# Kernel optimization log

Hardware: AMD Instinct MI355X
Metric: run time of the kernel (lower is better)

## Reference

```python
import jax, jax.numpy as jnp
import numpy as np

N, E, IN, HID, EE, L, NB = 20000, 256000, 64, 128, 32, 3, 8


def _silu(x):
    return x * jax.nn.sigmoid(x)


def setup_inputs() -> dict:
    key = jax.random.key(0)
    ks = list(jax.random.split(key, 32))

    def nrm(k, shape, fan_in):
        return jax.random.normal(k, shape, dtype=jnp.float32) / np.sqrt(fan_in)

    inp = {}
    inp["H_t"] = jax.random.normal(ks[0], (N, IN), dtype=jnp.float32)
    inp["X_t"] = jax.random.normal(ks[1], (N, 3), dtype=jnp.float32)
    inp["cond_embedding"] = jax.random.normal(ks[2], (N, HID), dtype=jnp.float32)
    inp["t"] = jax.random.uniform(ks[3], (N,), dtype=jnp.float32)
    inp["edges"] = jax.random.randint(ks[4], (2, E), 0, N)
    inp["edge_types"] = jax.random.randint(ks[5], (E,), 0, 2)
    inp["generate_mask"] = jax.random.bernoulli(ks[6], 0.7, (N,))
    inp["batch_ids"] = jnp.sort(jax.random.randint(ks[7], (N,), 0, NB))
    # input MLP: (IN + 2*HID) -> HID -> HID -> HID, 3 linear layers
    d0 = IN + 2 * HID
    inp["mlp_W0"] = nrm(ks[8], (d0, HID), d0)
    inp["mlp_b0"] = jnp.zeros((HID,), jnp.float32)
    inp["mlp_W1"] = nrm(ks[9], (HID, HID), HID)
    inp["mlp_b1"] = jnp.zeros((HID,), jnp.float32)
    inp["mlp_W2"] = nrm(ks[10], (HID, HID), HID)
    inp["mlp_b2"] = jnp.zeros((HID,), jnp.float32)
    inp["edge_table"] = jax.random.normal(ks[11], (2, EE), dtype=jnp.float32)
    # encoder (EGNN-style message passing), stacked over L layers
    de = 2 * HID + 1 + EE  # [h_src, h_dst, dist^2, edge_embed]
    inp["We"] = nrm(ks[12], (L, de, HID), de)
    inp["be"] = jnp.zeros((L, HID), jnp.float32)
    inp["Wx"] = nrm(ks[13], (L, HID, 1), HID)
    inp["bx"] = jnp.zeros((L, 1), jnp.float32)
    inp["Wh"] = nrm(ks[14], (L, 2 * HID, HID), 2 * HID)
    inp["bh"] = jnp.zeros((L, HID), jnp.float32)
    inp["h2i_W"] = nrm(ks[15], (HID, IN), HID)
    inp["h2i_b"] = jnp.zeros((IN,), jnp.float32)
    return inp


def reference(H_t, X_t, cond_embedding, t, mlp_W0, mlp_b0, mlp_W1, mlp_b1,
              mlp_W2, mlp_b2, edge_table, We, be, Wx, bx, Wh, bh,
              h2i_W, h2i_b, edges, edge_types, generate_mask, batch_ids):
    n = H_t.shape[0]
    hid = mlp_W2.shape[1]
    # sinusoidal time embedding (dim = hidden_size)
    half = hid // 2
    freqs = jnp.exp(jnp.arange(half, dtype=jnp.float32) * (-np.log(10000.0) / (half - 1)))
    ang = t[:, None] * freqs[None, :]
    t_embed = jnp.concatenate([jnp.sin(ang), jnp.cos(ang)], axis=-1)  # (N, hid)
    # input MLP
    feat = jnp.concatenate([H_t, cond_embedding, t_embed], axis=-1)
    h = jax.nn.relu(feat @ mlp_W0 + mlp_b0)
    h = jax.nn.relu(h @ mlp_W1 + mlp_b1)
    h = h @ mlp_W2 + mlp_b2
    eemb = edge_table[edge_types]  # (E, EE)
    src, dst = edges[0], edges[1]
    cnt = jax.ops.segment_sum(jnp.ones((src.shape[0], 1), h.dtype), dst, num_segments=n)
    x = X_t
    for l in range(We.shape[0]):
        diff = x[src] - x[dst]                              # (E, 3)
        d2 = jnp.sum(diff * diff, axis=-1, keepdims=True)   # (E, 1)
        m_in = jnp.concatenate([h[src], h[dst], d2, eemb], axis=-1)
        msg = _silu(m_in @ We[l] + be[l])                   # (E, hid)
        w = msg @ Wx[l] + bx[l]                             # (E, 1)
        agg_x = jax.ops.segment_sum(diff * w, dst, num_segments=n)
        x = x + agg_x / (cnt + 1.0)
        agg_m = jax.ops.segment_sum(msg, dst, num_segments=n)
        h = h + _silu(jnp.concatenate([h, agg_m], axis=-1) @ Wh[l] + bh[l])
    mask = generate_mask[:, None]
    v_X = jnp.where(mask, x, jnp.zeros_like(x))
    v_H = jnp.where(mask, h @ h2i_W + h2i_b, 0.0)
    return (v_H, v_X)
```

## Files before the change

### kernel.cpp

```cpp
#include <hip/hip_runtime.h>
#include <math.h>

#define NN 20000
#define NE 256000
#define IN_DIM 64
#define HID 128
#define DE 289
#define D0 320
#define TILE_E 64
#define NB64 313
#define NUB 8
#define SRCMASK 0x3FFFFFFF

typedef unsigned short u16;
typedef unsigned int u32;
typedef unsigned long long u64;
typedef __attribute__((ext_vector_type(8))) short short8;
typedef __attribute__((ext_vector_type(4))) float float4v;

#define OFF_WE   0
#define OFF_W0   122880
#define OFF_W1   163840
#define OFF_W2   180224
#define OFF_WH   196608
#define OFF_H2I  294912
#define PACK_TOT 303104
#define PREP_TOT (PACK_TOT + 1152 + NN)

static __device__ __forceinline__ u16 f2bf(float f) {
    unsigned int u = __float_as_uint(f);
    u += 0x7fffu + ((u >> 16) & 1u);
    return (u16)(u >> 16);
}
static __device__ __forceinline__ float bf2f(u16 s) {
    return __uint_as_float(((unsigned int)s) << 16);
}
static __device__ __forceinline__ float bflo(u32 u) { return bf2f((u16)(u & 0xffffu)); }
static __device__ __forceinline__ float bfhi(u32 u) { return bf2f((u16)(u >> 16)); }
static __device__ __forceinline__ u32 pack2(float a, float b) {
    return (u32)f2bf(a) | ((u32)f2bf(b) << 16);
}
static __device__ __forceinline__ uint4 pack8(const float* v) {
    uint4 r;
    r.x = (u32)f2bf(v[0]) | ((u32)f2bf(v[1]) << 16);
    r.y = (u32)f2bf(v[2]) | ((u32)f2bf(v[3]) << 16);
    r.z = (u32)f2bf(v[4]) | ((u32)f2bf(v[5]) << 16);
    r.w = (u32)f2bf(v[6]) | ((u32)f2bf(v[7]) << 16);
    return r;
}
static __device__ __forceinline__ float silu(float v) {
    return v * (1.f / (1.f + __expf(-v)));
}

__global__ __launch_bounds__(256) void hist_kernel(
    const float* __restrict__ X_t, const int* __restrict__ edges,
    float* __restrict__ x, int* __restrict__ deg)
{
    int gid = blockIdx.x * blockDim.x + threadIdx.x;
    int stride = gridDim.x * blockDim.x;
    for (int i = gid; i < NN * 3; i += stride) x[i] = X_t[i];
    for (int e = gid; e < NE; e += stride)
        atomicAdd(&deg[edges[NE + e]], 1);
}

__global__ __launch_bounds__(1024) void scan_kernel(
    const int* __restrict__ deg, int* __restrict__ row_start, int* __restrict__ head)
{
    __shared__ int s[1024];
    int tx = threadIdx.x;
    const int per = (NN + 1023) / 1024;
    int st = tx * per, en = st + per;
    if (st > NN) st = NN;
    if (en > NN) en = NN;
    int sum = 0;
    for (int i = st; i < en; ++i) sum += deg[i];
    s[tx] = sum;
    __syncthreads();
    for (int off = 1; off < 1024; off <<= 1) {
        int t = (tx >= off) ? s[tx - off] : 0;
        __syncthreads();
        s[tx] += t;
        __syncthreads();
    }
    int run = (tx == 0) ? 0 : s[tx - 1];
    for (int i = st; i < en; ++i) {
        row_start[i] = run; head[i] = run; run += deg[i];
    }
    if (tx == 1023) row_start[NN] = run;
}

__global__ __launch_bounds__(256) void scatter_kernel(
    const int* __restrict__ edges, const int* __restrict__ etype,
    int* __restrict__ head,
    int* __restrict__ src_s)
{
    int gid = blockIdx.x * blockDim.x + threadIdx.x;
    int stride = gridDim.x * blockDim.x;
    for (int e = gid; e < NE; e += stride) {
        int d = edges[NE + e];
        int p = atomicAdd(&head[d], 1);
        src_s[p] = edges[e] | (etype[e] << 30);
    }
}

__global__ __launch_bounds__(256) void prep_kernel(
    const float* __restrict__ We, const float* __restrict__ W0,
    const float* __restrict__ W1, const float* __restrict__ W2,
    const float* __restrict__ Wh, const float* __restrict__ h2i,
    const float* __restrict__ edge_table, const float* __restrict__ be,
    u16* __restrict__ Bp, float* __restrict__ tv, float* __restrict__ wed2,
    int* __restrict__ deg)
{
    int idx = blockIdx.x * 256 + threadIdx.x;
    if (idx < PACK_TOT) {
        const float* src; int N = 128, Ksrc; int r;
        if (idx < OFF_W0) {
            int layer = idx / 40960; r = idx - layer * 40960;
            src = We + (size_t)layer * DE * HID; Ksrc = DE;
        } else if (idx < OFF_W1) { r = idx - OFF_W0; src = W0; Ksrc = 320; }
        else if (idx < OFF_W2)   { r = idx - OFF_W1; src = W1; Ksrc = 128; }
        else if (idx < OFF_WH)   { r = idx - OFF_W2; src = W2; Ksrc = 128; }
        else if (idx < OFF_H2I) {
            int t = idx - OFF_WH; int layer = t / 32768; r = t - layer * 32768;
            src = Wh + (size_t)layer * 256 * HID; Ksrc = 256;
        } else { r = idx - OFF_H2I; src = h2i; Ksrc = 128; N = 64; }
        int ntc = N / 16;
        int j = r & 7, lane = (r >> 3) & 63;
        int rem = r >> 9;
        int nt = rem % ntc, ks = rem / ntc;
        int k = ks * 32 + ((lane >> 4) << 3) + j;
        int c = nt * 16 + (lane & 15);
        Bp[idx] = f2bf((k < Ksrc) ? src[(size_t)k * N + c] : 0.f);
    } else if (idx < PACK_TOT + 768) {
        int q = idx - PACK_TOT;
        int f = q & 127, t = (q >> 7) & 1, l = q >> 8;
        float acc = be[l * 128 + f];
        const float* W = We + (size_t)l * DE * HID;
        #pragma unroll
        for (int k = 0; k < 32; ++k)
            acc += edge_table[t * 32 + k] * W[(size_t)(257 + k) * HID + f];
        tv[l * 256 + t * 128 + f] = acc;
    } else if (idx < PACK_TOT + 1152) {
        int r = idx - PACK_TOT - 768;
        int f = r & 127, l = r >> 7;
        wed2[l * 128 + f] = We[(size_t)l * DE * HID + (size_t)256 * HID + f];
    } else if (idx < PREP_TOT) {
        deg[idx - PACK_TOT - 1152] = 0;
    }
}

__global__ __launch_bounds__(256) void node_mlp_mfma_kernel(
    const float* __restrict__ H_t, const float* __restrict__ cond,
    const float* __restrict__ t_in,
    const u16* __restrict__ W0p, const float* __restrict__ b0,
    const u16* __restrict__ W1p, const float* __restrict__ b1,
    const u16* __restrict__ W2p, const float* __restrict__ b2,
    const u16* __restrict__ WEp,
    u16* __restrict__ Csrc, u16* __restrict__ Cdst,
    float* __restrict__ h, u16* __restrict__ h_bf)
{
    __shared__ u16 s_A[64 * 64];
    __shared__ u16 s_B[64 * 128];
    __shared__ u16 s_h[64 * 128];
    __shared__ float s_t[64];

    int tx = threadIdx.x;
    int n0 = blockIdx.x * 64;
    int l = tx & 63, w = tx >> 6;
    int mt_base = (w & 1) * 2, nt_base = (w >> 1) * 4;
    const float cfr = -logf(10000.f) / 63.f;

    if (tx < 64) s_t[tx] = (n0 + tx < NN) ? t_in[n0 + tx] : 0.f;

    float4v acc[2][4];
    #pragma unroll
    for (int mi = 0; mi < 2; ++mi)
        #pragma unroll
        for (int ni = 0; ni < 4; ++ni) acc[mi][ni] = (float4v){0.f,0.f,0.f,0.f};

    for (int t = 0; t < 5; ++t) {
        __syncthreads();
        #pragma unroll
        for (int it = 0; it < 2; ++it) {
            int flat = it * 256 + tx;
            int n = flat >> 3, sl = flat & 7;
            int c = sl ^ (n & 7);
            int k0 = t * 64 + c * 8;
            float tv8[8];
            int gn = n0 + n;
            if (gn < NN) {
                if (k0 < 192) {
                    const float* src = (k0 < 64) ? &H_t[(size_t)gn * IN_DIM + k0]
                                                 : &cond[(size_t)gn * HID + (k0 - 64)];
                    float4 a = *(const float4*)src;
                    float4 b = *(const float4*)(src + 4);
                    tv8[0]=a.x; tv8[1]=a.y; tv8[2]=a.z; tv8[3]=a.w;
                    tv8[4]=b.x; tv8[5]=b.y; tv8[6]=b.z; tv8[7]=b.w;
                } else {
                    float tvv = s_t[n];
                    int jj = (k0 - 192) & 63;
                    bool is_sin = (k0 < 256);
                    #pragma unroll
                    for (int jx = 0; jx < 8; ++jx) {
                        float ang = tvv * __expf(cfr * (float)(jj + jx));
                        tv8[jx] = is_sin ? __sinf(ang) : __cosf(ang);
                    }
                }
            } else {
                #pragma unroll
                for (int jx = 0; jx < 8; ++jx) tv8[jx] = 0.f;
            }
            *(uint4*)&s_A[n * 64 + sl * 8] = pack8(tv8);
        }
        #pragma unroll
        for (int it = 0; it < 4; ++it) {
            int flat = it * 256 + tx;
            ((uint4*)s_B)[flat] = ((const uint4*)(W0p + (size_t)t * 8192))[flat];
        }
        __syncthreads();
        #pragma unroll
        for (int s = 0; s < 2; ++s) {
            short8 af[2], bfv[4];
            #pragma unroll
            for (int mi = 0; mi < 2; ++mi) {
                int m = (mt_base + mi) * 16 + (l & 15);
                int c = s * 4 + (l >> 4);
                int slot = c ^ (l & 7);
                af[mi] = *(const short8*)(s_A + m * 64 + slot * 8);
            }
            #pragma unroll
            for (int ni = 0; ni < 4; ++ni)
                bfv[ni] = *(const short8*)(s_B + ((s * 8 + nt_base + ni) * 64 + l) * 8);
            #pragma unroll
            for (int mi = 0; mi < 2; ++mi)
                #pragma unroll
                for (int ni = 0; ni < 4; ++ni)
                    acc[mi][ni] = __builtin_amdgcn_mfma_f32_16x16x32_bf16(
                        af[mi], bfv[ni], acc[mi][ni], 0, 0, 0);
        }
    }
    #pragma unroll
    for (int mi = 0; mi < 2; ++mi) {
        #pragma unroll
        for (int ni = 0; ni < 4; ++ni) {
            int f = (nt_base + ni) * 16 + (l & 15);
            float bv = b0[f];
            #pragma unroll
            for (int r = 0; r < 4; ++r) {
                int m = (mt_base + mi) * 16 + (l >> 4) * 4 + r;
                float v = fmaxf(acc[mi][ni][r] + bv, 0.f);
                int slot = (f >> 3) ^ (m & 7);
                s_h[m * 128 + slot * 8 + (f & 7)] = f2bf(v);
            }
            acc[mi][ni] = (float4v){0.f,0.f,0.f,0.f};
        }
    }
    for (int t = 0; t < 2; ++t) {
        __syncthreads();
        #pragma unroll
        for (int it = 0; it < 4; ++it) {
            int flat = it * 256 + tx;
            ((uint4*)s_B)[flat] = ((const uint4*)(W1p + (size_t)t * 8192))[flat];
        }
        __syncthreads();
        #pragma unroll
        for (int s = 0; s < 2; ++s) {
            short8 af[2], bfv[4];
            #pragma unroll
            for (int mi = 0; mi < 2; ++mi) {
                int m = (mt_base + mi) * 16 + (l & 15);
                int c = t * 8 + s * 4 + (l >> 4);
                int slot = c ^ (l & 7);
                af[mi] = *(const short8*)(s_h + m * 128 + slot * 8);
            }
            #pragma unroll
            for (int ni = 0; ni < 4; ++ni)
                bfv[ni] = *(const short8*)(s_B + ((s * 8 + nt_base + ni) * 64 + l) * 8);
            #pragma unroll
            for (int mi = 0; mi < 2; ++mi)
                #pragma unroll
                for (int ni = 0; ni < 4; ++ni)
                    acc[mi][ni] = __builtin_amdgcn_mfma_f32_16x16x32_bf16(
                        af[mi], bfv[ni], acc[mi][ni], 0, 0, 0);
        }
    }
    __syncthreads();
    #pragma unroll
    for (int mi = 0; mi < 2; ++mi) {
        #pragma unroll
        for (int ni = 0; ni < 4; ++ni) {
            int f = (nt_base + ni) * 16 + (l & 15);
            float bv = b1[f];
            #pragma unroll
            for (int r = 0; r < 4; ++r) {
                int m = (mt_base + mi) * 16 + (l >> 4) * 4 + r;
                float v = fmaxf(acc[mi][ni][r] + bv, 0.f);
                int slot = (f >> 3) ^ (m & 7);
                s_h[m * 128 + slot * 8 + (f & 7)] = f2bf(v);
            }
            acc[mi][ni] = (float4v){0.f,0.f,0.f,0.f};
        }
    }
    for (int t = 0; t < 2; ++t) {
        __syncthreads();
        #pragma unroll
        for (int it = 0; it < 4; ++it) {
            int flat = it * 256 + tx;
            ((uint4*)s_B)[flat] = ((const uint4*)(W2p + (size_t)t * 8192))[flat];
        }
        __syncthreads();
        #pragma unroll
        for (int s = 0; s < 2; ++s) {
            short8 af[2], bfv[4];
            #pragma unroll
            for (int mi = 0; mi < 2; ++mi) {
                int m = (mt_base + mi) * 16 + (l & 15);
                int c = t * 8 + s * 4 + (l >> 4);
                int slot = c ^ (l & 7);
                af[mi] = *(const short8*)(s_h + m * 128 + slot * 8);
            }
            #pragma unroll
            for (int ni = 0; ni < 4; ++ni)
                bfv[ni] = *(const short8*)(s_B + ((s * 8 + nt_base + ni) * 64 + l) * 8);
            #pragma unroll
            for (int mi = 0; mi < 2; ++mi)
                #pragma unroll
                for (int ni = 0; ni < 4; ++ni)
                    acc[mi][ni] = __builtin_amdgcn_mfma_f32_16x16x32_bf16(
                        af[mi], bfv[ni], acc[mi][ni], 0, 0, 0);
        }
    }
    __syncthreads();
    #pragma unroll
    for (int mi = 0; mi < 2; ++mi) {
        #pragma unroll
        for (int ni = 0; ni < 4; ++ni) {
            int f = (nt_base + ni) * 16 + (l & 15);
            float bv = b2[f];
            #pragma unroll
            for (int r = 0; r < 4; ++r) {
                int m = (mt_base + mi) * 16 + (l >> 4) * 4 + r;
                int gn = n0 + m;
                float v = acc[mi][ni][r] + bv;
                int slot = (f >> 3) ^ (m & 7);
                s_h[m * 128 + slot * 8 + (f & 7)] = f2bf(v);
                if (gn < NN) {
                    h[(size_t)gn * HID + f] = v;
                    h_bf[(size_t)gn * HID + f] = f2bf(v);
                }
            }
        }
    }

    for (int sd = 0; sd < 2; ++sd) {
        #pragma unroll
        for (int mi = 0; mi < 2; ++mi)
            #pragma unroll
            for (int ni = 0; ni < 4; ++ni) acc[mi][ni] = (float4v){0.f,0.f,0.f,0.f};
        #pragma unroll
        for (int th = 0; th < 2; ++th) {
            int t = sd * 2 + th;
            __syncthreads();
            #pragma unroll
            for (int it = 0; it < 4; ++it) {
                int flat = it * 256 + tx;
                ((uint4*)s_B)[flat] = ((const uint4*)(WEp + (size_t)t * 8192))[flat];
            }
            __syncthreads();
            #pragma unroll
            for (int s = 0; s < 2; ++s) {
                short8 af[2], bfv[4];
                #pragma unroll
                for (int mi = 0; mi < 2; ++mi) {
                    int m = (mt_base + mi) * 16 + (l & 15);
                    int c = th * 8 + s * 4 + (l >> 4);
                    int slot = c ^ (l & 7);
                    af[mi] = *(const short8*)(s_h + m * 128 + slot * 8);
                }
                #pragma unroll
                for (int ni = 0; ni < 4; ++ni)
                    bfv[ni] = *(const short8*)(s_B + ((s * 8 + nt_base + ni) * 64 + l) * 8);
                #pragma unroll
                for (int mi = 0; mi < 2; ++mi)
                    #pragma unroll
                    for (int ni = 0; ni < 4; ++ni)
                        acc[mi][ni] = __builtin_amdgcn_mfma_f32_16x16x32_bf16(
                            af[mi], bfv[ni], acc[mi][ni], 0, 0, 0);
            }
        }
        u16* Cout = (sd == 0) ? Csrc : Cdst;
        #pragma unroll
        for (int mi = 0; mi < 2; ++mi) {
            #pragma unroll
            for (int ni = 0; ni < 4; ++ni) {
                int fq = (nt_base + ni) * 16 + (l & 15);
                #pragma unroll
                for (int r = 0; r < 4; ++r) {
                    int m = (mt_base + mi) * 16 + (l >> 4) * 4 + r;
                    int gn = n0 + m;
                    if (gn < NN)
                        Cout[(size_t)gn * 128 + fq] = f2bf(acc[mi][ni][r]);
                }
            }
        }
    }
}

__global__ __launch_bounds__(512, 4) void node_fused_kernel(
    float* __restrict__ h, u16* __restrict__ h_bf,
    const float* __restrict__ x_in, float* __restrict__ x_out,
    const u16* __restrict__ Csrc, const u16* __restrict__ Cdst,
    u16* __restrict__ Csrc_n, u16* __restrict__ Cdst_n,
    const u16* __restrict__ Wnext, const float* __restrict__ bfin,
    const int* __restrict__ gmask, float* __restrict__ out,
    const int* __restrict__ src_s,
    const int* __restrict__ row_start,
    const float* __restrict__ tv_l, const float* __restrict__ wed2_l,
    const float* __restrict__ Wx_l, const float* __restrict__ bx_l,
    const u16* __restrict__ Whp_l, const float* __restrict__ bh_l,
    int mode)
{
    __shared__ u16 s_A[16 * 256];
    __shared__ u16 s_h2[16 * 128];

    int tx = threadIdx.x;
    int n0 = blockIdx.x * NUB;
    int l = tx & 63, w = tx >> 6;
    int i = w;
    int gn = n0 + i;
    int p = l & 31, q = l >> 5;

    if (tx < 256) {
        int n = tx >> 4, c = tx & 15;
        int slot = c ^ (n & 7);
        uint4 v = make_uint4(0, 0, 0, 0);
        if (n < NUB) v = *(const uint4*)(h_bf + (size_t)(n0 + n) * 128 + c * 8);
        *(uint4*)&s_A[n * 256 + slot * 8] = v;
    } else if (tx < 384) {
        int n = 8 + ((tx - 256) >> 4), c = 16 + (tx & 15);
        int slot = c ^ (n & 7);
        *(uint4*)&s_A[n * 256 + slot * 8] = make_uint4(0, 0, 0, 0);
    }

    float c0[4], d01[4], wed[4], wx[4];
    {
        uint2 cd = *(const uint2*)(Cdst + (size_t)gn * 128 + p * 4);
        float cdv0 = bflo(cd.x), cdv1 = bfhi(cd.x), cdv2 = bflo(cd.y), cdv3 = bfhi(cd.y);
        float4 t0 = *(const float4*)(tv_l + p * 4);
        float4 t1 = *(const float4*)(tv_l + 128 + p * 4);
        float4 wd = *(const float4*)(wed2_l + p * 4);
        float4 wv = *(const float4*)(Wx_l + p * 4);
        c0[0] = t0.x + cdv0; c0[1] = t0.y + cdv1; c0[2] = t0.z + cdv2; c0[3] = t0.w + cdv3;
        d01[0] = t1.x - t0.x; d01[1] = t1.y - t0.y; d01[2] = t1.z - t0.z; d01[3] = t1.w - t0.w;
        wed[0] = wd.x; wed[1] = wd.y; wed[2] = wd.z; wed[3] = wd.w;
        wx[0] = wv.x; wx[1] = wv.y; wx[2] = wv.z; wx[3] = wv.w;
    }
    float bx32 = bx_l[0] * (1.f / 32.f);

    int rs = row_start[gn], re = row_start[gn + 1];
    int d = re - rs;

    float xd0 = x_in[gn * 3 + 0], xd1 = x_in[gn * 3 + 1], xd2 = x_in[gn * 3 + 2];

    float ag[4] = {0.f, 0.f, 0.f, 0.f};
    float sx = 0.f, sy = 0.f, sz = 0.f;

    for (int e0 = 0; e0 < d; e0 += 64) {
        int nchunk = d - e0; if (nchunk > 64) nchunk = 64;
        int sp_l = (l < nchunk) ? src_s[rs + e0 + l] : 0;
        float gx_l = 0.f, gy_l = 0.f, gz_l = 0.f, d2_l = 0.f;
        if (l < nchunk) {
            int sm = sp_l & SRCMASK;
            gx_l = x_in[sm * 3 + 0] - xd0;
            gy_l = x_in[sm * 3 + 1] - xd1;
            gz_l = x_in[sm * 3 + 2] - xd2;
            d2_l = gx_l * gx_l + gy_l * gy_l + gz_l * gz_l;
        }

        auto FETCH = [&](int lj, uint2& cc, float& et) {
            int spE = __shfl(sp_l, lj);
            cc = make_uint2(0u, 0u); et = 0.f;
            if (lj < nchunk) {
                cc = *(const uint2*)(Csrc + (size_t)(spE & SRCMASK) * 128 + p * 4);
                et = (float)((u32)spE >> 30);
            }
        };
        auto PROC = [&](int lj, uint2 cc, float ee) {
            float dxe = __shfl(gx_l, lj);
            float dye = __shfl(gy_l, lj);
            float dze = __shfl(gz_l, lj);
            float d2e = __shfl(d2_l, lj);
            float av[4];
            av[0] = bflo(cc.x); av[1] = bfhi(cc.x);
            av[2] = bflo(cc.y); av[3] = bfhi(cc.y);
            float wpart = bx32;
            #pragma unroll
            for (int f = 0; f < 4; ++f) {
                float t = __fmaf_rn(d2e, wed[f], c0[f]);
                t = __fmaf_rn(ee, d01[f], t);
                float v = av[f] + t;
                float m = silu(v);
                ag[f] += m;
                wpart = __fmaf_rn(m, wx[f], wpart);
            }
            sx = __fmaf_rn(dxe, wpart, sx);
            sy = __fmaf_rn(dye, wpart, sy);
            sz = __fmaf_rn(dze, wpart, sz);
        };

        int ljA = q, ljB = q + 2, ljC = q + 4, ljD = q + 6, ljn = q + 8;
        uint2 ccA, ccB, ccC, ccD; float etA, etB, etC, etD;
        FETCH(ljA, ccA, etA); FETCH(ljB, ccB, etB);
        FETCH(ljC, ccC, etC); FETCH(ljD, ccD, etD);
        while (ljA < nchunk) {
            PROC(ljA, ccA, etA); ljA = ljn; ljn += 2; FETCH(ljA, ccA, etA);
            if (ljB >= nchunk) break;
            PROC(ljB, ccB, etB); ljB = ljn; ljn += 2; FETCH(ljB, ccB, etB);
            if (ljC >= nchunk) break;
            PROC(ljC, ccC, etC); ljC = ljn; ljn += 2; FETCH(ljC, ccC, etC);
            if (ljD >= nchunk) break;
            PROC(ljD, ccD, etD); ljD = ljn; ljn += 2; FETCH(ljD, ccD, etD);
        }
    }

    #pragma unroll
    for (int f = 0; f < 4; ++f) ag[f] += __shfl_xor(ag[f], 32);
    #pragma unroll
    for (int off = 1; off <= 32; off <<= 1) {
        sx += __shfl_xor(sx, off);
        sy += __shfl_xor(sy, off);
        sz += __shfl_xor(sz, off);
    }
    if (l < 32) {
        int c2 = 16 + (p >> 1);
        int slot = c2 ^ (i & 7);
        uint2 o;
        o.x = pack2(ag[0], ag[1]);
        o.y = pack2(ag[2], ag[3]);
        *(uint2*)&s_A[i * 256 + slot * 8 + (p & 1) * 4] = o;
    }
    float inv = 1.f / ((float)d + 1.f);
    if (l == 0) {
        x_out[gn * 3 + 0] = xd0 + sx * inv;
        x_out[gn * 3 + 1] = xd1 + sy * inv;
        x_out[gn * 3 + 2] = xd2 + sz * inv;
    }
    if (mode == 1 && l < 3) {
        float xv = (l == 0) ? (xd0 + sx * inv)
                 : (l == 1) ? (xd1 + sy * inv)
                            : (xd2 + sz * inv);
        out[(size_t)NN * IN_DIM + gn * 3 + l] = gmask[gn] ? xv : 0.f;
    }

    __syncthreads();

    float4v acc = (float4v){0.f, 0.f, 0.f, 0.f};
    #pragma unroll
    for (int t = 0; t < 4; ++t) {
        #pragma unroll
        for (int s = 0; s < 2; ++s) {
            int m = l & 15;
            int c = t * 8 + s * 4 + (l >> 4);
            int slot = c ^ (l & 7);
            short8 af = *(const short8*)(s_A + m * 256 + slot * 8);
            short8 bfv = *(const short8*)(Whp_l + (size_t)t * 8192 + ((s * 8 + w) * 64 + l) * 8);
            acc = __builtin_amdgcn_mfma_f32_16x16x32_bf16(af, bfv, acc, 0, 0, 0);
        }
    }
    {
        int f = w * 16 + (l & 15);
        float bv = bh_l[f];
        #pragma unroll
        for (int r = 0; r < 4; ++r) {
            int m = (l >> 4) * 4 + r;
            u16 hb = 0;
            if (m < NUB) {
                int gn2 = n0 + m;
                float v = acc[r] + bv;
                float hn = h[(size_t)gn2 * HID + f] + silu(v);
                hb = f2bf(hn);
                if (mode == 0) {
                    h[(size_t)gn2 * HID + f] = hn;
                    h_bf[(size_t)gn2 * HID + f] = hb;
                }
            }
            int slot2 = (f >> 3) ^ (m & 7);
            s_h2[m * 128 + slot2 * 8 + (f & 7)] = hb;
        }
    }
    __syncthreads();

    if (mode == 0) {
        #pragma unroll
        for (int j = 0; j < 2; ++j) {
            int g = w * 2 + j;
            int sd = g >> 3, nt = g & 7;
            float4v a2 = (float4v){0.f, 0.f, 0.f, 0.f};
            #pragma unroll
            for (int kt = 0; kt < 2; ++kt) {
                #pragma unroll
                for (int s = 0; s < 2; ++s) {
                    int c = kt * 8 + s * 4 + (l >> 4);
                    int slot = c ^ (l & 7);
                    short8 af = *(const short8*)(s_h2 + (l & 15) * 128 + slot * 8);
                    short8 bfv = *(const short8*)(Wnext + (size_t)(sd * 2 + kt) * 8192
                                                  + ((s * 8 + nt) * 64 + l) * 8);
                    a2 = __builtin_amdgcn_mfma_f32_16x16x32_bf16(af, bfv, a2, 0, 0, 0);
                }
            }
            u16* Cout = sd ? Cdst_n : Csrc_n;
            int f = nt * 16 + (l & 15);
            #pragma unroll
            for (int r = 0; r < 4; ++r) {
                int m = (l >> 4) * 4 + r;
                if (m < NUB)
                    Cout[(size_t)(n0 + m) * 128 + f] = f2bf(a2[r]);
            }
        }
    } else {
        if (w < 4) {
            int nt = w;
            float4v a2 = (float4v){0.f, 0.f, 0.f, 0.f};
            #pragma unroll
            for (int t = 0; t < 2; ++t) {
                #pragma unroll
                for (int s = 0; s < 2; ++s) {
                    int c = t * 8 + s * 4 + (l >> 4);
                    int slot = c ^ (l & 7);
                    short8 af = *(const short8*)(s_h2 + (l & 15) * 128 + slot * 8);
                    short8 bfv = *(const short8*)(Wnext + (size_t)t * 4096
                                                  + ((s * 4 + nt) * 64 + l) * 8);
                    a2 = __builtin_amdgcn_mfma_f32_16x16x32_bf16(af, bfv, a2, 0, 0, 0);
                }
            }
            int f = nt * 16 + (l & 15);
            float bv = bfin[f];
            #pragma unroll
            for (int r = 0; r < 4; ++r) {
                int m = (l >> 4) * 4 + r;
                if (m < NUB) {
                    int gn2 = n0 + m;
                    out[(size_t)gn2 * IN_DIM + f] = gmask[gn2] ? (a2[r] + bv) : 0.f;
                }
            }
        }
    }
}

__global__ __launch_bounds__(256) void init_fb_kernel(
    const float* __restrict__ X_t, const int* __restrict__ edges,
    float* __restrict__ x, float* __restrict__ cnt)
{
    int gid = blockIdx.x * blockDim.x + threadIdx.x;
    int stride = gridDim.x * blockDim.x;
    for (int i = gid; i < NN * 3; i += stride) x[i] = X_t[i];
    for (int e = gid; e < NE; e += stride)
        atomicAdd(&cnt[edges[NE + e]], 1.0f);
}

__global__ __launch_bounds__(128) void node_mlp_kernel(
    const float* __restrict__ H_t, const float* __restrict__ cond,
    const float* __restrict__ t_in,
    const float* __restrict__ W0, const float* __restrict__ b0,
    const float* __restrict__ W1, const float* __restrict__ b1,
    const float* __restrict__ W2, const float* __restrict__ b2,
    float* __restrict__ h)
{
    __shared__ float s_feat[D0][20];
    __shared__ float s_h0[HID][20];
    __shared__ float s_h1[HID][20];
    int n0 = blockIdx.x * 16;
    int tx = threadIdx.x;

    for (int idx = tx; idx < 16 * IN_DIM; idx += 128) {
        int i = idx >> 6, k = idx & 63;
        s_feat[k][i] = H_t[(n0 + i) * IN_DIM + k];
    }
    for (int idx = tx; idx < 16 * HID; idx += 128) {
        int i = idx >> 7, k = idx & 127;
        s_feat[IN_DIM + k][i] = cond[(n0 + i) * HID + k];
    }
    const float cfr = -logf(10000.f) / 63.f;
    for (int idx = tx; idx < 16 * HID; idx += 128) {
        int i = idx >> 7, k = idx & 127;
        float tv = t_in[n0 + i];
        int jj = k & 63;
        float ang = tv * __expf(cfr * (float)jj);
        s_feat[IN_DIM + HID + k][i] = (k < 64) ? __sinf(ang) : __cosf(ang);
    }
    __syncthreads();

    float acc[16];
    {
        float bv = b0[tx];
        #pragma unroll
        for (int i = 0; i < 16; ++i) acc[i] = bv;
        for (int k = 0; k < D0; ++k) {
            float w = W0[k * HID + tx];
            float4 f0 = *(const float4*)&s_feat[k][0];
            float4 f1 = *(const float4*)&s_feat[k][4];
            float4 f2 = *(const float4*)&s_feat[k][8];
            float4 f3 = *(const float4*)&s_feat[k][12];
            acc[0] += f0.x*w; acc[1] += f0.y*w; acc[2] += f0.z*w; acc[3] += f0.w*w;
            acc[4] += f1.x*w; acc[5] += f1.y*w; acc[6] += f1.z*w; acc[7] += f1.w*w;
            acc[8] += f2.x*w; acc[9] += f2.y*w; acc[10]+= f2.z*w; acc[11]+= f2.w*w;
            acc[12]+= f3.x*w; acc[13]+= f3.y*w; acc[14]+= f3.z*w; acc[15]+= f3.w*w;
        }
        #pragma unroll
        for (int i = 0; i < 16; ++i) s_h0[tx][i] = fmaxf(acc[i], 0.f);
    }
    __syncthreads();
    {
        float bv = b1[tx];
        #pragma unroll
        for (int i = 0; i < 16; ++i) acc[i] = bv;
        for (int k = 0; k < HID; ++k) {
            float w = W1[k * HID + tx];
            float4 f0 = *(const float4*)&s_h0[k][0];
            float4 f1 = *(const float4*)&s_h0[k][4];
            float4 f2 = *(const float4*)&s_h0[k][8];
            float4 f3 = *(const float4*)&s_h0[k][12];
            acc[0] += f0.x*w; acc[1] += f0.y*w; acc[2] += f0.z*w; acc[3] += f0.w*w;
            acc[4] += f1.x*w; acc[5] += f1.y*w; acc[6] += f1.z*w; acc[7] += f1.w*w;
            acc[8] += f2.x*w; acc[9] += f2.y*w; acc[10]+= f2.z*w; acc[11]+= f2.w*w;
            acc[12]+= f3.x*w; acc[13]+= f3.y*w; acc[14]+= f3.z*w; acc[15]+= f3.w*w;
        }
        #pragma unroll
        for (int i = 0; i < 16; ++i) s_h1[tx][i] = fmaxf(acc[i], 0.f);
    }
    __syncthreads();
    {
        float bv = b2[tx];
        #pragma unroll
        for (int i = 0; i < 16; ++i) acc[i] = bv;
        for (int k = 0; k < HID; ++k) {
            float w = W2[k * HID + tx];
            float4 f0 = *(const float4*)&s_h1[k][0];
            float4 f1 = *(const float4*)&s_h1[k][4];
            float4 f2 = *(const float4*)&s_h1[k][8];
            float4 f3 = *(const float4*)&s_h1[k][12];
            acc[0] += f0.x*w; acc[1] += f0.y*w; acc[2] += f0.z*w; acc[3] += f0.w*w;
            acc[4] += f1.x*w; acc[5] += f1.y*w; acc[6] += f1.z*w; acc[7] += f1.w*w;
            acc[8] += f2.x*w; acc[9] += f2.y*w; acc[10]+= f2.z*w; acc[11]+= f2.w*w;
            acc[12]+= f3.x*w; acc[13]+= f3.y*w; acc[14]+= f3.z*w; acc[15]+= f3.w*w;
        }
        #pragma unroll
        for (int i = 0; i < 16; ++i) h[(n0 + i) * HID + tx] = acc[i];
    }
}

__global__ __launch_bounds__(256) void edge_gemm_fb_kernel(
    const float* __restrict__ h, const float* __restrict__ x,
    const int* __restrict__ edges, const int* __restrict__ etype,
    const float* __restrict__ edge_table,
    const float* __restrict__ We_l, const float* __restrict__ be_l,
    const float* __restrict__ Wx_l, const float* __restrict__ bx_l,
    float* __restrict__ agg_m, float* __restrict__ agg_x)
{
    __shared__ int s_src[TILE_E], s_dst[TILE_E];
    __shared__ float s_diff[TILE_E][3];
    __shared__ float s_tail[TILE_E][36];
    __shared__ float s_Af[TILE_E][36];
    __shared__ float s_Bf[33][HID];
    __shared__ float s_wx[HID];

    int e0 = blockIdx.x * TILE_E;
    int tx = threadIdx.x;
    int tf = tx & 15;
    int te = tx >> 4;

    if (tx < TILE_E) {
        int s = edges[e0 + tx];
        int d = edges[NE + e0 + tx];
        s_src[tx] = s; s_dst[tx] = d;
        float dx = x[s * 3 + 0] - x[d * 3 + 0];
        float dy = x[s * 3 + 1] - x[d * 3 + 1];
        float dz = x[s * 3 + 2] - x[d * 3 + 2];
        s_diff[tx][0] = dx; s_diff[tx][1] = dy; s_diff[tx][2] = dz;
        s_tail[tx][0] = dx * dx + dy * dy + dz * dz;
        int et = etype[e0 + tx];
        #pragma unroll
        for (int j = 0; j < 32; ++j) s_tail[tx][1 + j] = edge_table[et * 32 + j];
    }
    if (tx < HID) s_wx[tx] = Wx_l[tx];
    __syncthreads();

    float acc[4][8];
    #pragma unroll
    for (int i = 0; i < 4; ++i)
        #pragma unroll
        for (int j = 0; j < 8; ++j) acc[i][j] = 0.f;

    for (int t = 0; t < 9; ++t) {
        int k0 = t * 32;
        int klen = (t == 8) ? 33 : 32;
        __syncthreads();
        if (t < 8) {
            const bool use_src = (t < 4);
            int kbase = (t & 3) * 32;
            for (int q4 = tx; q4 < TILE_E * 8; q4 += 256) {
                int e = q4 >> 3, q = q4 & 7;
                int row = use_src ? s_src[e] : s_dst[e];
                float4 v = *(const float4*)&h[row * HID + kbase + q * 4];
                *(float4*)&s_Af[e][q * 4] = v;
            }
        }
        for (int q4 = tx; q4 < klen * 32; q4 += 256) {
            int kk = q4 >> 5, c4 = q4 & 31;
            float4 v = *(const float4*)&We_l[(k0 + kk) * HID + c4 * 4];
            *(float4*)&s_Bf[kk][c4 * 4] = v;
        }
        __syncthreads();
        const float (*Asrc)[36] = (t == 8) ? (const float (*)[36])s_tail
                                           : (const float (*)[36])s_Af;
        for (int kk = 0; kk < klen; ++kk) {
            float a0 = Asrc[te * 4 + 0][kk];
            float a1 = Asrc[te * 4 + 1][kk];
            float a2 = Asrc[te * 4 + 2][kk];
            float a3 = Asrc[te * 4 + 3][kk];
            float4 bv0 = *(const float4*)&s_Bf[kk][tf * 8];
            float4 bv1 = *(const float4*)&s_Bf[kk][tf * 8 + 4];
            float b[8] = {bv0.x, bv0.y, bv0.z, bv0.w, bv1.x, bv1.y, bv1.z, bv1.w};
            #pragma unroll
            for (int j = 0; j < 8; ++j) {
                acc[0][j] += a0 * b[j];
                acc[1][j] += a1 * b[j];
                acc[2][j] += a2 * b[j];
                acc[3][j] += a3 * b[j];
            }
        }
    }

    float wsum[4];
    #pragma unroll
    for (int i = 0; i < 4; ++i) {
        float p = 0.f;
        #pragma unroll
        for (int j = 0; j < 8; ++j) {
            int f = tf * 8 + j;
            float v = acc[i][j] + be_l[f];
            float m = silu(v);
            acc[i][j] = m;
            p += m * s_wx[f];
        }
        wsum[i] = p;
    }
    #pragma unroll
    for (int off = 1; off < 16; off <<= 1) {
        #pragma unroll
        for (int i = 0; i < 4; ++i) wsum[i] += __shfl_xor(wsum[i], off);
    }
    float bxv = bx_l[0];
    if (tf < 3) {
        #pragma unroll
        for (int i = 0; i < 4; ++i) {
            int e = te * 4 + i;
            float w2 = wsum[i] + bxv;
            atomicAdd(&agg_x[s_dst[e] * 3 + tf], s_diff[e][tf] * w2);
        }
    }
    #pragma unroll
    for (int i = 0; i < 4; ++i) {
        int d = s_dst[te * 4 + i];
        #pragma unroll
        for (int j = 0; j < 8; ++j)
            atomicAdd(&agg_m[d * HID + tf * 8 + j], acc[i][j]);
    }
}

__global__ __launch_bounds__(128) void node_update_fb_kernel(
    float* __restrict__ h, float* __restrict__ x,
    const float* __restrict__ agg_m, const float* __restrict__ agg_x,
    const float* __restrict__ cnt,
    const float* __restrict__ Wh_l, const float* __restrict__ bh_l)
{
    __shared__ float s_in[256][20];
    int n0 = blockIdx.x * 16;
    int tx = threadIdx.x;
    for (int idx = tx; idx < 16 * HID; idx += 128) {
        int i = idx >> 7, k = idx & 127;
        s_in[k][i] = h[(n0 + i) * HID + k];
    }
    for (int idx = tx; idx < 16 * HID; idx += 128) {
        int i = idx >> 7, k = idx & 127;
        s_in[HID + k][i] = agg_m[(n0 + i) * HID + k];
    }
    __syncthreads();
    float acc[16];
    float bv = bh_l[tx];
    #pragma unroll
    for (int i = 0; i < 16; ++i) acc[i] = bv;
    for (int k = 0; k < 256; ++k) {
        float w = Wh_l[k * HID + tx];
        float4 f0 = *(const float4*)&s_in[k][0];
        float4 f1 = *(const float4*)&s_in[k][4];
        float4 f2 = *(const float4*)&s_in[k][8];
        float4 f3 = *(const float4*)&s_in[k][12];
        acc[0] += f0.x*w; acc[1] += f0.y*w; acc[2] += f0.z*w; acc[3] += f0.w*w;
        acc[4] += f1.x*w; acc[5] += f1.y*w; acc[6] += f1.z*w; acc[7] += f1.w*w;
        acc[8] += f2.x*w; acc[9] += f2.y*w; acc[10]+= f2.z*w; acc[11]+= f2.w*w;
        acc[12]+= f3.x*w; acc[13]+= f3.y*w; acc[14]+= f3.z*w; acc[15]+= f3.w*w;
    }
    #pragma unroll
    for (int i = 0; i < 16; ++i) {
        float v = acc[i];
        h[(n0 + i) * HID + tx] = s_in[tx][i] + silu(v);
    }
    if (tx < 48) {
        int i = tx / 3, c = tx % 3;
        int n = n0 + i;
        x[n * 3 + c] += agg_x[n * 3 + c] / (cnt[n] + 1.f);
    }
}

__global__ __launch_bounds__(64) void final_fb_kernel(
    const float* __restrict__ h, const float* __restrict__ x,
    const int* __restrict__ gmask,
    const float* __restrict__ W, const float* __restrict__ b,
    float* __restrict__ out)
{
    __shared__ float s_h[8][HID];
    int n0 = blockIdx.x * 8;
    int tx = threadIdx.x;
    for (int idx = tx; idx < 8 * HID; idx += 64) {
        int i = idx >> 7, k = idx & 127;
        s_h[i][k] = h[(n0 + i) * HID + k];
    }
    __syncthreads();
    float acc[8];
    float bv = b[tx];
    #pragma unroll
    for (int i = 0; i < 8; ++i) acc[i] = bv;
    for (int k = 0; k < HID; ++k) {
        float w = W[k * IN_DIM + tx];
        #pragma unroll
        for (int i = 0; i < 8; ++i) acc[i] += s_h[i][k] * w;
    }
    #pragma unroll
    for (int i = 0; i < 8; ++i) {
        int n = n0 + i;
        out[n * IN_DIM + tx] = gmask[n] ? acc[i] : 0.f;
    }
    if (tx < 24) {
        int i = tx / 3, c = tx % 3;
        int n = n0 + i;
        out[NN * IN_DIM + n * 3 + c] = gmask[n] ? x[n * 3 + c] : 0.f;
    }
}

extern "C" void kernel_launch(void* const* d_in, const int* in_sizes, int n_in,
                              void* d_out, int out_size, void* d_ws, size_t ws_size,
                              hipStream_t stream) {
    const float* H_t   = (const float*)d_in[0];
    const float* X_t   = (const float*)d_in[1];
    const float* cond  = (const float*)d_in[2];
    const float* t_in  = (const float*)d_in[3];
    const int*   edges = (const int*)d_in[4];
    const int*   etype = (const int*)d_in[5];
    const int*   gmask = (const int*)d_in[6];
    const float* W0 = (const float*)d_in[8];
    const float* b0 = (const float*)d_in[9];
    const float* W1 = (const float*)d_in[10];
    const float* b1 = (const float*)d_in[11];
    const float* W2 = (const float*)d_in[12];
    const float* b2 = (const float*)d_in[13];
    const float* edge_table = (const float*)d_in[14];
    const float* We = (const float*)d_in[15];
    const float* be = (const float*)d_in[16];
    const float* Wx = (const float*)d_in[17];
    const float* bx = (const float*)d_in[18];
    const float* Wh = (const float*)d_in[19];
    const float* bh = (const float*)d_in[20];
    const float* h2i_W = (const float*)d_in[21];
    const float* h2i_b = (const float*)d_in[22];

    char* p = (char*)d_ws;
    float* h = (float*)p;           p += (size_t)NN * HID * 4;
    u16* h_bf = (u16*)p;            p += (size_t)NN * HID * 2;
    float* xa = (float*)p;          p += (size_t)NN * 3 * 4;
    float* xb = (float*)p;          p += (size_t)NN * 3 * 4;
    u16* Ca_s = (u16*)p;            p += (size_t)NN * 128 * 2;
    u16* Ca_d = (u16*)p;            p += (size_t)NN * 128 * 2;
    u16* Cb_s = (u16*)p;            p += (size_t)NN * 128 * 2;
    u16* Cb_d = (u16*)p;            p += (size_t)NN * 128 * 2;
    u16* Bpack = (u16*)p;           p += (size_t)PACK_TOT * 2;
    float* tv = (float*)p;          p += (size_t)768 * 4;
    float* wed2 = (float*)p;        p += (size_t)384 * 4;
    int* row_start = (int*)p;       p += (size_t)(NN + 4) * 4;
    int* deg = (int*)p;             p += (size_t)NN * 4;
    int* head = (int*)p;            p += (size_t)NN * 4;
    int* src_s = (int*)p;           p += (size_t)NE * 4;
    size_t need = (size_t)(p - (char*)d_ws);

    if (ws_size >= need) {
        prep_kernel<<<(PREP_TOT + 255) / 256, 256, 0, stream>>>(
            We, W0, W1, W2, Wh, h2i_W, edge_table, be, Bpack, tv, wed2, deg);
        hist_kernel<<<256, 256, 0, stream>>>(X_t, edges, xa, deg);
        scan_kernel<<<1, 1024, 0, stream>>>(deg, row_start, head);
        scatter_kernel<<<256, 256, 0, stream>>>(edges, etype, head, src_s);
        node_mlp_mfma_kernel<<<NB64, 256, 0, stream>>>(
            H_t, cond, t_in,
            Bpack + OFF_W0, b0, Bpack + OFF_W1, b1, Bpack + OFF_W2, b2,
            Bpack + OFF_WE, Ca_s, Ca_d,
            h, h_bf);
        for (int l = 0; l < 3; ++l) {
            const float* xin = (l & 1) ? xb : xa;
            float* xout = (l & 1) ? xa : xb;
            const u16* cs_in = (l & 1) ? Cb_s : Ca_s;
            const u16* cd_in = (l & 1) ? Cb_d : Ca_d;
            u16* cs_out = (l & 1) ? Ca_s : Cb_s;
            u16* cd_out = (l & 1) ? Ca_d : Cb_d;
            int mode = (l == 2) ? 1 : 0;
            const u16* Wnext = mode ? (Bpack + OFF_H2I)
                                    : (Bpack + OFF_WE + (size_t)(l + 1) * 40960);
            node_fused_kernel<<<NN / NUB, 512, 0, stream>>>(
                h, h_bf, xin, xout, cs_in, cd_in, cs_out, cd_out,
                Wnext, h2i_b, gmask, (float*)d_out,
                src_s, row_start,
                tv + (size_t)l * 256, wed2 + (size_t)l * 128,
                Wx + l * HID, bx + l,
                Bpack + OFF_WH + (size_t)l * 32768, bh + l * HID,
                mode);
        }
    } else {
        float* ws    = (float*)d_ws;
        float* fh    = ws;
        float* fx    = fh + NN * HID;
        float* cnt   = fx + NN * 3;
        float* fagg_m = cnt + NN;
        float* fagg_x = fagg_m + NN * HID;

        hipMemsetAsync(cnt, 0, NN * sizeof(float), stream);
        init_fb_kernel<<<256, 256, 0, stream>>>(X_t, edges, fx, cnt);
        node_mlp_kernel<<<NN / 16, 128, 0, stream>>>(H_t, cond, t_in,
                                                     W0, b0, W1, b1, W2, b2, fh);
        for (int l = 0; l < 3; ++l) {
            hipMemsetAsync(fagg_m, 0, (size_t)NN * 131 * sizeof(float), stream);
            edge_gemm_fb_kernel<<<NE / TILE_E, 256, 0, stream>>>(
                fh, fx, edges, etype, edge_table,
                We + (size_t)l * DE * HID, be + l * HID,
                Wx + l * HID, bx + l, fagg_m, fagg_x);
            node_update_fb_kernel<<<NN / 16, 128, 0, stream>>>(
                fh, fx, fagg_m, fagg_x, cnt,
                Wh + (size_t)l * 256 * HID, bh + l * HID);
        }
        final_fb_kernel<<<NN / 8, 64, 0, stream>>>(fh, fx, gmask, h2i_W, h2i_b, (float*)d_out);
    }
}
```

Measured before the change: 353.6 us.

## Process 16 nodes per block and parallelize the degree prefix scan

Result: faster. 298.4 us (median of 2 runs) (-15.6%).

```diff
diff --git a/kernel.cpp b/kernel.cpp
--- a/kernel.cpp
+++ b/kernel.cpp
@@ -9,7 +9,8 @@
 #define D0 320
 #define TILE_E 64
 #define NB64 313
-#define NUB 8
+#define NUB 16
+#define SCB 79
 #define SRCMASK 0x3FFFFFFF
 
 typedef unsigned short u16;
@@ -63,30 +64,52 @@
         atomicAdd(&deg[edges[NE + e]], 1);
 }
 
-__global__ __launch_bounds__(1024) void scan_kernel(
-    const int* __restrict__ deg, int* __restrict__ row_start, int* __restrict__ head)
-{
-    __shared__ int s[1024];
-    int tx = threadIdx.x;
-    const int per = (NN + 1023) / 1024;
-    int st = tx * per, en = st + per;
-    if (st > NN) st = NN;
-    if (en > NN) en = NN;
-    int sum = 0;
-    for (int i = st; i < en; ++i) sum += deg[i];
-    s[tx] = sum;
-    __syncthreads();
-    for (int off = 1; off < 1024; off <<= 1) {
-        int t = (tx >= off) ? s[tx - off] : 0;
-        __syncthreads();
-        s[tx] += t;
-        __syncthreads();
-    }
-    int run = (tx == 0) ? 0 : s[tx - 1];
-    for (int i = st; i < en; ++i) {
-        row_start[i] = run; head[i] = run; run += deg[i];
-    }
-    if (tx == 1023) row_start[NN] = run;
+__global__ __launch_bounds__(256) void scan1_kernel(
+    const int* __restrict__ deg, int* __restrict__ row_start, int* __restrict__ bsum)
+{
+    __shared__ int s[256];
+    int t = threadIdx.x;
+    int n = blockIdx.x * 256 + t;
+    int v = (n < NN) ? deg[n] : 0;
+    s[t] = v;
+    __syncthreads();
+    for (int off = 1; off < 256; off <<= 1) {
+        int u = (t >= off) ? s[t - off] : 0;
+        __syncthreads();
+        s[t] += u;
+        __syncthreads();
+    }
+    if (n < NN) row_start[n] = s[t] - v;
+    if (t == 255) bsum[blockIdx.x] = s[255];
+}
+
+__global__ __launch_bounds__(128) void scan2_kernel(
+    int* __restrict__ bsum, int* __restrict__ row_start)
+{
+    __shared__ int s[128];
+    int t = threadIdx.x;
+    int v = (t < SCB) ? bsum[t] : 0;
+    s[t] = v;
+    __syncthreads();
+    for (int off = 1; off < 128; off <<= 1) {
+        int u = (t >= off) ? s[t - off] : 0;
+        __syncthreads();
+        s[t] += u;
+        __syncthreads();
+    }
+    if (t < SCB) bsum[t] = s[t] - v;
+    if (t == SCB - 1) row_start[NN] = s[t];
+}
+
+__global__ __launch_bounds__(256) void scan3_kernel(
+    int* __restrict__ row_start, const int* __restrict__ bsum, int* __restrict__ head)
+{
+    int n = blockIdx.x * 256 + threadIdx.x;
+    if (n < NN) {
+        int v = row_start[n] + bsum[blockIdx.x];
+        row_start[n] = v;
+        head[n] = v;
+    }
 }
 
 __global__ __launch_bounds__(256) void scatter_kernel(
@@ -426,130 +449,132 @@
     int tx = threadIdx.x;
     int n0 = blockIdx.x * NUB;
     int l = tx & 63, w = tx >> 6;
-    int i = w;
-    int gn = n0 + i;
     int p = l & 31, q = l >> 5;
 
     if (tx < 256) {
         int n = tx >> 4, c = tx & 15;
         int slot = c ^ (n & 7);
-        uint4 v = make_uint4(0, 0, 0, 0);
-        if (n < NUB) v = *(const uint4*)(h_bf + (size_t)(n0 + n) * 128 + c * 8);
+        uint4 v = *(const uint4*)(h_bf + (size_t)(n0 + n) * 128 + c * 8);
         *(uint4*)&s_A[n * 256 + slot * 8] = v;
-    } else if (tx < 384) {
-        int n = 8 + ((tx - 256) >> 4), c = 16 + (tx & 15);
-        int slot = c ^ (n & 7);
-        *(uint4*)&s_A[n * 256 + slot * 8] = make_uint4(0, 0, 0, 0);
-    }
-
-    float c0[4], d01[4], wed[4], wx[4];
+    }
+
+    float tva[4], d01[4], wed[4], wx[4];
     {
-        uint2 cd = *(const uint2*)(Cdst + (size_t)gn * 128 + p * 4);
-        float cdv0 = bflo(cd.x), cdv1 = bfhi(cd.x), cdv2 = bflo(cd.y), cdv3 = bfhi(cd.y);
         float4 t0 = *(const float4*)(tv_l + p * 4);
         float4 t1 = *(const float4*)(tv_l + 128 + p * 4);
         float4 wd = *(const float4*)(wed2_l + p * 4);
         float4 wv = *(const float4*)(Wx_l + p * 4);
-        c0[0] = t0.x + cdv0; c0[1] = t0.y + cdv1; c0[2] = t0.z + cdv2; c0[3] = t0.w + cdv3;
+        tva[0] = t0.x; tva[1] = t0.y; tva[2] = t0.z; tva[3] = t0.w;
         d01[0] = t1.x - t0.x; d01[1] = t1.y - t0.y; d01[2] = t1.z - t0.z; d01[3] = t1.w - t0.w;
         wed[0] = wd.x; wed[1] = wd.y; wed[2] = wd.z; wed[3] = wd.w;
         wx[0] = wv.x; wx[1] = wv.y; wx[2] = wv.z; wx[3] = wv.w;
     }
     float bx32 = bx_l[0] * (1.f / 32.f);
 
-    int rs = row_start[gn], re = row_start[gn + 1];
-    int d = re - rs;
-
-    float xd0 = x_in[gn * 3 + 0], xd1 = x_in[gn * 3 + 1], xd2 = x_in[gn * 3 + 2];
-
-    float ag[4] = {0.f, 0.f, 0.f, 0.f};
-    float sx = 0.f, sy = 0.f, sz = 0.f;
-
-    for (int e0 = 0; e0 < d; e0 += 64) {
-        int nchunk = d - e0; if (nchunk > 64) nchunk = 64;
-        int sp_l = (l < nchunk) ? src_s[rs + e0 + l] : 0;
-        float gx_l = 0.f, gy_l = 0.f, gz_l = 0.f, d2_l = 0.f;
-        if (l < nchunk) {
-            int sm = sp_l & SRCMASK;
-            gx_l = x_in[sm * 3 + 0] - xd0;
-            gy_l = x_in[sm * 3 + 1] - xd1;
-            gz_l = x_in[sm * 3 + 2] - xd2;
-            d2_l = gx_l * gx_l + gy_l * gy_l + gz_l * gz_l;
-        }
-
-        auto FETCH = [&](int lj, uint2& cc, float& et) {
-            int spE = __shfl(sp_l, lj);
-            cc = make_uint2(0u, 0u); et = 0.f;
-            if (lj < nchunk) {
-                cc = *(const uint2*)(Csrc + (size_t)(spE & SRCMASK) * 128 + p * 4);
-                et = (float)((u32)spE >> 30);
-            }
-        };
-        auto PROC = [&](int lj, uint2 cc, float ee) {
-            float dxe = __shfl(gx_l, lj);
-            float dye = __shfl(gy_l, lj);
-            float dze = __shfl(gz_l, lj);
-            float d2e = __shfl(d2_l, lj);
-            float av[4];
-            av[0] = bflo(cc.x); av[1] = bfhi(cc.x);
-            av[2] = bflo(cc.y); av[3] = bfhi(cc.y);
-            float wpart = bx32;
-            #pragma unroll
-            for (int f = 0; f < 4; ++f) {
-                float t = __fmaf_rn(d2e, wed[f], c0[f]);
-                t = __fmaf_rn(ee, d01[f], t);
-                float v = av[f] + t;
-                float m = silu(v);
-                ag[f] += m;
-                wpart = __fmaf_rn(m, wx[f], wpart);
-            }
-            sx = __fmaf_rn(dxe, wpart, sx);
-            sy = __fmaf_rn(dye, wpart, sy);
-            sz = __fmaf_rn(dze, wpart, sz);
-        };
-
-        int ljA = q, ljB = q + 2, ljC = q + 4, ljD = q + 6, ljn = q + 8;
-        uint2 ccA, ccB, ccC, ccD; float etA, etB, etC, etD;
-        FETCH(ljA, ccA, etA); FETCH(ljB, ccB, etB);
-        FETCH(ljC, ccC, etC); FETCH(ljD, ccD, etD);
-        while (ljA < nchunk) {
-            PROC(ljA, ccA, etA); ljA = ljn; ljn += 2; FETCH(ljA, ccA, etA);
-            if (ljB >= nchunk) break;
-            PROC(ljB, ccB, etB); ljB = ljn; ljn += 2; FETCH(ljB, ccB, etB);
-            if (ljC >= nchunk) break;
-            PROC(ljC, ccC, etC); ljC = ljn; ljn += 2; FETCH(ljC, ccC, etC);
-            if (ljD >= nchunk) break;
-            PROC(ljD, ccD, etD); ljD = ljn; ljn += 2; FETCH(ljD, ccD, etD);
-        }
-    }
-
-    #pragma unroll
-    for (int f = 0; f < 4; ++f) ag[f] += __shfl_xor(ag[f], 32);
-    #pragma unroll
-    for (int off = 1; off <= 32; off <<= 1) {
-        sx += __shfl_xor(sx, off);
-        sy += __shfl_xor(sy, off);
-        sz += __shfl_xor(sz, off);
-    }
-    if (l < 32) {
-        int c2 = 16 + (p >> 1);
-        int slot = c2 ^ (i & 7);
-        uint2 o;
-        o.x = pack2(ag[0], ag[1]);
-        o.y = pack2(ag[2], ag[3]);
-        *(uint2*)&s_A[i * 256 + slot * 8 + (p & 1) * 4] = o;
-    }
-    float inv = 1.f / ((float)d + 1.f);
-    if (l == 0) {
-        x_out[gn * 3 + 0] = xd0 + sx * inv;
-        x_out[gn * 3 + 1] = xd1 + sy * inv;
-        x_out[gn * 3 + 2] = xd2 + sz * inv;
-    }
-    if (mode == 1 && l < 3) {
-        float xv = (l == 0) ? (xd0 + sx * inv)
-                 : (l == 1) ? (xd1 + sy * inv)
-                            : (xd2 + sz * inv);
-        out[(size_t)NN * IN_DIM + gn * 3 + l] = gmask[gn] ? xv : 0.f;
+    #pragma unroll
+    for (int nn = 0; nn < 2; ++nn) {
+        int i2 = 2 * w + nn;
+        int gn = n0 + i2;
+
+        float c0[4];
+        {
+            uint2 cd = *(const uint2*)(Cdst + (size_t)gn * 128 + p * 4);
+            c0[0] = tva[0] + bflo(cd.x); c0[1] = tva[1] + bfhi(cd.x);
+            c0[2] = tva[2] + bflo(cd.y); c0[3] = tva[3] + bfhi(cd.y);
+        }
+        int rs = row_start[gn], re = row_start[gn + 1];
+        int d = re - rs;
+        float xd0 = x_in[gn * 3 + 0], xd1 = x_in[gn * 3 + 1], xd2 = x_in[gn * 3 + 2];
+
+        float ag[4] = {0.f, 0.f, 0.f, 0.f};
+        float sx = 0.f, sy = 0.f, sz = 0.f;
+
+        for (int e0 = 0; e0 < d; e0 += 64) {
+            int nchunk = d - e0; if (nchunk > 64) nchunk = 64;
+            int sp_l = (l < nchunk) ? src_s[rs + e0 + l] : 0;
+            float gx_l = 0.f, gy_l = 0.f, gz_l = 0.f, d2_l = 0.f;
+            if (l < nchunk) {
+                int sm = sp_l & SRCMASK;
+                gx_l = x_in[sm * 3 + 0] - xd0;
+                gy_l = x_in[sm * 3 + 1] - xd1;
+                gz_l = x_in[sm * 3 + 2] - xd2;
+                d2_l = gx_l * gx_l + gy_l * gy_l + gz_l * gz_l;
+            }
+
+            auto FETCH = [&](int lj, uint2& cc, float& et) {
+                int spE = __shfl(sp_l, lj);
+                cc = make_uint2(0u, 0u); et = 0.f;
+                if (lj < nchunk) {
+                    cc = *(const uint2*)(Csrc + (size_t)(spE & SRCMASK) * 128 + p * 4);
+                    et = (float)((u32)spE >> 30);
+                }
+            };
+            auto PROC = [&](int lj, uint2 cc, float ee) {
+                float dxe = __shfl(gx_l, lj);
+                float dye = __shfl(gy_l, lj);
+                float dze = __shfl(gz_l, lj);
+                float d2e = __shfl(d2_l, lj);
+                float av[4];
+                av[0] = bflo(cc.x); av[1] = bfhi(cc.x);
+                av[2] = bflo(cc.y); av[3] = bfhi(cc.y);
+                float wpart = bx32;
+                #pragma unroll
+                for (int f = 0; f < 4; ++f) {
+                    float t = __fmaf_rn(d2e, wed[f], c0[f]);
+                    t = __fmaf_rn(ee, d01[f], t);
+                    float v = av[f] + t;
+                    float m = silu(v);
+                    ag[f] += m;
+                    wpart = __fmaf_rn(m, wx[f], wpart);
+                }
+                sx = __fmaf_rn(dxe, wpart, sx);
+                sy = __fmaf_rn(dye, wpart, sy);
+                sz = __fmaf_rn(dze, wpart, sz);
+            };
+
+            int ljA = q, ljB = q + 2, ljC = q + 4, ljD = q + 6, ljn = q + 8;
+            uint2 ccA, ccB, ccC, ccD; float etA, etB, etC, etD;
+            FETCH(ljA, ccA, etA); FETCH(ljB, ccB, etB);
+            FETCH(ljC, ccC, etC); FETCH(ljD, ccD, etD);
+            while (ljA < nchunk) {
+                PROC(ljA, ccA, etA); ljA = ljn; ljn += 2; FETCH(ljA, ccA, etA);
+                if (ljB >= nchunk) break;
+                PROC(ljB, ccB, etB); ljB = ljn; ljn += 2; FETCH(ljB, ccB, etB);
+                if (ljC >= nchunk) break;
+                PROC(ljC, ccC, etC); ljC = ljn; ljn += 2; FETCH(ljC, ccC, etC);
+                if (ljD >= nchunk) break;
+                PROC(ljD, ccD, etD); ljD = ljn; ljn += 2; FETCH(ljD, ccD, etD);
+            }
+        }
+
+        #pragma unroll
+        for (int f = 0; f < 4; ++f) ag[f] += __shfl_xor(ag[f], 32);
+        #pragma unroll
+        for (int off = 1; off <= 32; off <<= 1) {
+            sx += __shfl_xor(sx, off);
+            sy += __shfl_xor(sy, off);
+            sz += __shfl_xor(sz, off);
+        }
+        if (l < 32) {
+            int c2 = 16 + (p >> 1);
+            int slot = c2 ^ (i2 & 7);
+            uint2 o;
+            o.x = pack2(ag[0], ag[1]);
+            o.y = pack2(ag[2], ag[3]);
+            *(uint2*)&s_A[i2 * 256 + slot * 8 + (p & 1) * 4] = o;
+        }
+        float inv = 1.f / ((float)d + 1.f);
+        if (l == 0) {
+            x_out[gn * 3 + 0] = xd0 + sx * inv;
+            x_out[gn * 3 + 1] = xd1 + sy * inv;
+            x_out[gn * 3 + 2] = xd2 + sz * inv;
+        }
+        if (mode == 1 && l < 3) {
+            float xv = (l == 0) ? (xd0 + sx * inv)
+                     : (l == 1) ? (xd1 + sy * inv)
+                                : (xd2 + sz * inv);
+            out[(size_t)NN * IN_DIM + gn * 3 + l] = gmask[gn] ? xv : 0.f;
+        }
     }
 
     __syncthreads();
@@ -573,16 +598,13 @@
         #pragma unroll
         for (int r = 0; r < 4; ++r) {
             int m = (l >> 4) * 4 + r;
-            u16 hb = 0;
-            if (m < NUB) {
-                int gn2 = n0 + m;
-                float v = acc[r] + bv;
-                float hn = h[(size_t)gn2 * HID + f] + silu(v);
-                hb = f2bf(hn);
-                if (mode == 0) {
-                    h[(size_t)gn2 * HID + f] = hn;
-                    h_bf[(size_t)gn2 * HID + f] = hb;
-                }
+            int gn2 = n0 + m;
+            float v = acc[r] + bv;
+            float hn = h[(size_t)gn2 * HID + f] + silu(v);
+            u16 hb = f2bf(hn);
+            if (mode == 0) {
+                h[(size_t)gn2 * HID + f] = hn;
+                h_bf[(size_t)gn2 * HID + f] = hb;
             }
             int slot2 = (f >> 3) ^ (m & 7);
             s_h2[m * 128 + slot2 * 8 + (f & 7)] = hb;
@@ -613,8 +635,7 @@
             #pragma unroll
             for (int r = 0; r < 4; ++r) {
                 int m = (l >> 4) * 4 + r;
-                if (m < NUB)
-                    Cout[(size_t)(n0 + m) * 128 + f] = f2bf(a2[r]);
+                Cout[(size_t)(n0 + m) * 128 + f] = f2bf(a2[r]);
             }
         }
     } else {
@@ -638,10 +659,8 @@
             #pragma unroll
             for (int r = 0; r < 4; ++r) {
                 int m = (l >> 4) * 4 + r;
-                if (m < NUB) {
-                    int gn2 = n0 + m;
-                    out[(size_t)gn2 * IN_DIM + f] = gmask[gn2] ? (a2[r] + bv) : 0.f;
-                }
+                int gn2 = n0 + m;
+                out[(size_t)gn2 * IN_DIM + f] = gmask[gn2] ? (a2[r] + bv) : 0.f;
             }
         }
     }
@@ -989,6 +1008,7 @@
     int* row_start = (int*)p;       p += (size_t)(NN + 4) * 4;
     int* deg = (int*)p;             p += (size_t)NN * 4;
     int* head = (int*)p;            p += (size_t)NN * 4;
+    int* bsum = (int*)p;            p += (size_t)128 * 4;
     int* src_s = (int*)p;           p += (size_t)NE * 4;
     size_t need = (size_t)(p - (char*)d_ws);
 
@@ -996,7 +1016,9 @@
         prep_kernel<<<(PREP_TOT + 255) / 256, 256, 0, stream>>>(
             We, W0, W1, W2, Wh, h2i_W, edge_table, be, Bpack, tv, wed2, deg);
         hist_kernel<<<256, 256, 0, stream>>>(X_t, edges, xa, deg);
-        scan_kernel<<<1, 1024, 0, stream>>>(deg, row_start, head);
+        scan1_kernel<<<SCB, 256, 0, stream>>>(deg, row_start, bsum);
+        scan2_kernel<<<1, 128, 0, stream>>>(bsum, row_start);
+        scan3_kernel<<<SCB, 256, 0, stream>>>(row_start, bsum, head);
         scatter_kernel<<<256, 256, 0, stream>>>(edges, etype, head, src_s);
         node_mlp_mfma_kernel<<<NB64, 256, 0, stream>>>(
             H_t, cond, t_in,
```
